# Kernel optimization log

Measured on AMD Instinct MI355X. Metric: run time of the kernel, lower is better.

Reference implementation:

```python
import jax, jax.numpy as jnp
import numpy as np

D = 100        # persistence-image resolution (forced by CNN out: 32*25*25)
VAR = 0.5      # pers_im_var
B, P = 32, 128 # graphs, persistence pairs per graph
N, IN, HID = 16000, 128, 64
NUM_CLASSES = 10


def setup_inputs() -> dict:
    key = jax.random.key(0)
    ks = jax.random.split(key, 13)
    s = 0.05
    return {
        "x": jax.random.normal(ks[0], (N, IN), jnp.float32),
        "pair_idx0": jax.random.randint(ks[1], (B, P, 2), 0, N, jnp.int32),
        "pair_idx1": jax.random.randint(ks[2], (B, P, 2), 0, N, jnp.int32),
        "w1": jax.random.normal(ks[3], (IN, HID), jnp.float32) * s,
        "b1": jnp.zeros((HID,), jnp.float32),
        "w2": jax.random.normal(ks[4], (HID, 1), jnp.float32) * s,
        "b2": jnp.zeros((1,), jnp.float32),
        "conv1_w": jax.random.normal(ks[5], (16, 2, 5, 5), jnp.float32) * s,
        "conv1_b": jnp.zeros((16,), jnp.float32),
        "conv2_w": jax.random.normal(ks[6], (32, 16, 5, 5), jnp.float32) * s,
        "conv2_b": jnp.zeros((32,), jnp.float32),
        "out_w": jax.random.normal(ks[7], (NUM_CLASSES, 32 * 25 * 25), jnp.float32) * s,
        "out_b": jnp.zeros((NUM_CLASSES,), jnp.float32),
    }


def _pers_image(bd):
    # bd: [B, P, 2] birth/death filtration values
    # bdpt_to_bdps = [[1,-1],[0,1]] : (b, d) -> (b, d - b)
    birth = bd[..., 0]
    pers = bd[..., 1] - bd[..., 0]
    coords = jnp.arange(D, dtype=bd.dtype) / D  # arange(0, 0.999, 1/D) -> D pts
    # Gaussian over 2D grid; axis i <-> birth coord, axis j <-> persistence coord
    g = (birth[:, :, None, None] - coords[None, None, :, None]) ** 2 \
        + (pers[:, :, None, None] - coords[None, None, None, :]) ** 2
    im = jnp.exp(-g / (2.0 * VAR)) / (2.0 * jnp.pi * VAR)  # [B, P, D, D]
    im = im.sum(axis=1)  # sum over points -> [B, D, D]
    im = im / im.max(axis=(1, 2), keepdims=True)  # per-sample normalization
    return im


def _conv(x, w, b):
    y = jax.lax.conv_general_dilated(
        x, w, window_strides=(1, 1), padding=((2, 2), (2, 2)),
        dimension_numbers=("NCHW", "OIHW", "NCHW"))
    return y + b[None, :, None, None]


def _maxpool2(x):
    return jax.lax.reduce_window(x, -jnp.inf, jax.lax.max,
                                 (1, 1, 2, 2), (1, 1, 2, 2), "VALID")


def reference(x, pair_idx0, pair_idx1, w1, b1, w2, b2,
              conv1_w, conv1_b, conv2_w, conv2_b, out_w, out_b):
    # Linear_fil: Linear -> ReLU -> Linear -> Sigmoid -> squeeze
    h = jax.nn.relu(x @ w1 + b1)
    node_filt = jax.nn.sigmoid(h @ w2 + b2)[:, 0]  # [N]

    # persistence pairs as gathers of vertex filtration values (diff. path of ph)
    h0 = node_filt[pair_idx0]  # [B, P, 2]
    h1 = node_filt[pair_idx1]  # [B, P, 2]

    im0 = _pers_image(h0)
    im1 = _pers_image(h1)
    imgs = jnp.stack([im0, im1], axis=1)  # [B, 2, D, D]

    # CNN head
    y = _maxpool2(jax.nn.relu(_conv(imgs, conv1_w, conv1_b)))  # [B,16,50,50]
    y = _maxpool2(jax.nn.relu(_conv(y, conv2_w, conv2_b)))     # [B,32,25,25]
    y = y.reshape(y.shape[0], -1)
    y_hat = y @ out_w.T + out_b  # [B, num_classes]
    return (y_hat, node_filt)
```

## Files before the change

kernel.cpp:

```cpp
#include <hip/hip_runtime.h>
#include <hip/hip_bf16.h>

#define N_NODES 16000
#define IN_F 128
#define HID 64
#define BATCH 32
#define NPAIR 128
#define DRES 100
#define NCLS 10

#define NF_OFF     0
#define WA1_OFF    16000
#define WT2B_OFF   16800
#define INV_OFF    23200
#define MAXB_OFF   23264
#define IMGSP_OFF  23328
#define POOL1P_OFF 715552
#define POOL2_OFF  2263840
#define ZERO_N4    560144

#define NFILT_BLK  125
#define NZBLK      548

typedef short short8 __attribute__((ext_vector_type(8)));
typedef float f32x16 __attribute__((ext_vector_type(16)));

static __device__ __forceinline__ unsigned short f2b(float f) {
    __hip_bfloat16 h = __float2bfloat16(f);
    return *reinterpret_cast<unsigned short*>(&h);
}
static __device__ __forceinline__ unsigned int pk2(float a, float b) {
    return (unsigned int)f2b(a) | ((unsigned int)f2b(b) << 16);
}

#define COFF(k) (((k)/25)*336 + (((k)%25)/5)*56 + ((k)%25)%5)
#define C1OFF(k) ((k) < 50 ? ((k)/25)*624 + ((((k)%25)/5))*104 + (((k)%25)%5) : 1248)

__global__ __launch_bounds__(256) void k_initfilt(
    const float* __restrict__ x, const float* __restrict__ w1,
    const float* __restrict__ b1, const float* __restrict__ w2,
    const float* __restrict__ b2, float* __restrict__ nf, float* __restrict__ out_nf,
    const float* __restrict__ c1w, const float* __restrict__ c2w,
    unsigned int* __restrict__ wA1, unsigned int* __restrict__ wT2b,
    float* __restrict__ zbase)
{
    int bx = blockIdx.x, t = threadIdx.x;
    if (bx < NFILT_BLK) {
        int wave = t >> 6, lane = t & 63;
        int n0 = (bx * 4 + wave) * 32;
        int hh = lane >> 5, sm = lane & 31;
        const float* xr = x + (size_t)(n0 + sm) * IN_F + hh * 8;
        const float* wbase = w1 + hh * 512 + sm;

        f32x16 acc0 = {0.f,0.f,0.f,0.f,0.f,0.f,0.f,0.f,0.f,0.f,0.f,0.f,0.f,0.f,0.f,0.f};
        f32x16 acc1 = {0.f,0.f,0.f,0.f,0.f,0.f,0.f,0.f,0.f,0.f,0.f,0.f,0.f,0.f,0.f,0.f};

        #pragma unroll
        for (int s = 0; s < 8; ++s) {
            float4 v0 = *(const float4*)(xr + s * 16);
            float4 v1 = *(const float4*)(xr + s * 16 + 4);
            union { short8 v; unsigned int u[4]; } a;
            a.u[0] = pk2(v0.x, v0.y);
            a.u[1] = pk2(v0.z, v0.w);
            a.u[2] = pk2(v1.x, v1.y);
            a.u[3] = pk2(v1.z, v1.w);
            union { short8 v; unsigned int u[4]; } b0f, b1f;
            #pragma unroll
            for (int r = 0; r < 4; ++r) {
                float wa0 = wbase[s * 1024 + r * 128];
                float wb0 = wbase[s * 1024 + r * 128 + 64];
                float wa1 = wbase[s * 1024 + r * 128 + 32];
                float wb1v = wbase[s * 1024 + r * 128 + 96];
                b0f.u[r] = pk2(wa0, wb0);
                b1f.u[r] = pk2(wa1, wb1v);
            }
            acc0 = __builtin_amdgcn_mfma_f32_32x32x16_bf16(a.v, b0f.v, acc0, 0, 0, 0);
            acc1 = __builtin_amdgcn_mfma_f32_32x32x16_bf16(a.v, b1f.v, acc1, 0, 0, 0);
        }

        int h0 = sm, h1 = 32 + sm;
        float b10 = b1[h0], b11 = b1[h1], w20 = w2[h0], w21 = w2[h1];
        float q[16];
        #pragma unroll
        for (int r = 0; r < 16; ++r)
            q[r] = fmaxf(acc0[r] + b10, 0.f) * w20 + fmaxf(acc1[r] + b11, 0.f) * w21;
        #pragma unroll
        for (int off = 1; off < 32; off <<= 1) {
            #pragma unroll
            for (int r = 0; r < 16; ++r)
                q[r] += __shfl_xor(q[r], off, 64);
        }
        if (sm == 0) {
            float b2v = b2[0];
            #pragma unroll
            for (int r = 0; r < 16; ++r) {
                int m = (r & 3) + 8 * (r >> 2) + 4 * hh;
                float f = 1.f / (1.f + expf(-(q[r] + b2v)));
                nf[n0 + m] = f;
                out_nf[n0 + m] = f;
            }
        }
        return;
    }
    if (bx == NFILT_BLK) {
        for (int i = t; i < 512; i += 256) {
            int r = i & 3, m = (i >> 2) & 15, kg = (i >> 6) & 1, s = i >> 7;
            int k0 = s * 16 + kg * 8 + 2 * r;
            float f0 = (k0 < 50) ? c1w[m * 50 + k0] : 0.f;
            float f1 = (k0 + 1 < 50) ? c1w[m * 50 + k0 + 1] : 0.f;
            wA1[i] = pk2(f0, f1);
        }
        return;
    }
    if (bx == NFILT_BLK + 1) {
        for (int i = t; i < 6400; i += 256) {
            int kp = i >> 5, oc = i & 31;
            int k0 = 2 * kp, k1 = k0 + 1;
            float f0 = c2w[(oc * 16 + k0 / 25) * 25 + k0 % 25];
            float f1 = c2w[(oc * 16 + k1 / 25) * 25 + k1 % 25];
            wT2b[i] = pk2(f0, f1);
        }
        return;
    }
    int zi = (bx - (NFILT_BLK + 2)) * 1024 + t;
    float4 z = make_float4(0.f, 0.f, 0.f, 0.f);
    #pragma unroll
    for (int r = 0; r < 4; ++r) {
        int i = zi + r * 256;
        if (i < ZERO_N4) ((float4*)zbase)[i] = z;
    }
}

__global__ __launch_bounds__(256) void k_pimg(const float* __restrict__ nf,
    const int* __restrict__ pi0, const int* __restrict__ pi1,
    float* __restrict__ imgs_p, unsigned int* __restrict__ maxb)
{
    int g = blockIdx.x;
    int img = (g & 7) * 8 + ((g >> 3) & 7);
    int q = g >> 6;
    int b = img >> 1, c = img & 1;
    const int* pi = c ? pi1 : pi0;
    __shared__ float sb[NPAIR], sp[NPAIR];
    __shared__ float wm[4];
    int t = threadIdx.x;
    if (t < NPAIR) {
        int i0 = pi[(b * NPAIR + t) * 2 + 0];
        int i1 = pi[(b * NPAIR + t) * 2 + 1];
        float f0 = nf[i0], f1 = nf[i1];
        sb[t] = f0;
        sp[t] = f1 - f0;
    }
    __syncthreads();
    bool act = t < 169;
    int ti = t / 13, tj = t % 13;
    float acc[8][2] = {};
    if (act) {
        float ci[8];
        #pragma unroll
        for (int r = 0; r < 8; ++r) ci[r] = (float)(ti + 13 * r) * 0.01f;
        float cj0 = (float)(q * 25 + tj) * 0.01f;
        float cj1 = (float)(q * 25 + tj + 13) * 0.01f;
        for (int p = 0; p < NPAIR; ++p) {
            float bb = sb[p], pp = sp[p];
            float d0 = pp - cj0, d1 = pp - cj1;
            float e0 = __expf(-d0 * d0), e1 = __expf(-d1 * d1);
            #pragma unroll
            for (int r = 0; r < 8; ++r) {
                float d = bb - ci[r];
                float eb = __expf(-d * d);
                acc[r][0] = fmaf(eb, e0, acc[r][0]);
                acc[r][1] = fmaf(eb, e1, acc[r][1]);
            }
        }
    }
    float lmax = 0.f;
    if (act) {
        float* dst = imgs_p + (size_t)img * 10816 + 2 * 104 + 2 + q * 25;
        #pragma unroll
        for (int r = 0; r < 8; ++r) {
            int i = ti + 13 * r;
            if (i < DRES) {
                dst[i * 104 + tj] = acc[r][0];
                lmax = fmaxf(lmax, acc[r][0]);
                if (tj < 12) {
                    dst[i * 104 + tj + 13] = acc[r][1];
                    lmax = fmaxf(lmax, acc[r][1]);
                }
            }
        }
    }
    #pragma unroll
    for (int off = 32; off > 0; off >>= 1)
        lmax = fmaxf(lmax, __shfl_xor(lmax, off, 64));
    if ((t & 63) == 0) wm[t >> 6] = lmax;
    __syncthreads();
    if (t == 0) {
        float bm = fmaxf(fmaxf(wm[0], wm[1]), fmaxf(wm[2], wm[3]));
        atomicMax(&maxb[img], __float_as_uint(bm));
    }
}

__global__ __launch_bounds__(128) void k_conv1(const float* __restrict__ imgs_p,
    const unsigned int* __restrict__ wA1, const float* __restrict__ cb1,
    const unsigned int* __restrict__ maxb, float* __restrict__ pool1p)
{
    int g = blockIdx.x;
    int b = (g & 7) * 4 + ((g >> 3) & 3);
    int py = g >> 5;
    int t = threadIdx.x;

    __shared__ unsigned short inbz[1472];
    {
        float sc0 = 1.f / __uint_as_float(maxb[b * 2 + 0]);
        float sc1 = 1.f / __uint_as_float(maxb[b * 2 + 1]);
        const float* s0 = imgs_p + (size_t)(b * 2 + 0) * 10816 + (2 * py) * 104;
        const float* s1 = s0 + 10816;
        unsigned int* z32 = (unsigned int*)inbz;
        for (int i = t; i < 736; i += 128) {
            unsigned int val = 0u;
            if (i < 312) {
                int s2 = 2 * i; int r = s2 / 104, cc = s2 % 104;
                float2 v = *(const float2*)(s0 + r * 104 + cc);
                val = pk2(v.x * sc0, v.y * sc0);
            } else if (i < 624) {
                int s2 = 2 * i - 624; int r = s2 / 104, cc = s2 % 104;
                float2 v = *(const float2*)(s1 + r * 104 + cc);
                val = pk2(v.x * sc1, v.y * sc1);
            }
            z32[i] = val;
        }
    }
    __syncthreads();

    int lane = t & 63;
    int h = t >> 6;
    int hh = lane >> 5;
    int sm = lane & 31;
    int q = lane & 3;
    int cl = sm >> 2;
    int laneoff = (q >> 1) * 104 + 2 * cl + (q & 1);

    uint4 z4 = {0u, 0u, 0u, 0u};
    union { short8 v; uint4 qd; } afr[4];
    #pragma unroll
    for (int s = 0; s < 4; ++s)
        afr[s].qd = (sm < 16) ? *(const uint4*)(wA1 + ((s * 2 + hh) * 16 + sm) * 4) : z4;

    float bb[8];
    #pragma unroll
    for (int r = 0; r < 8; ++r)
        bb[r] = cb1[(r & 3) + 8 * (r >> 2) + 4 * hh];

    #pragma unroll
    for (int tt = 0; tt < 4; ++tt) {
        int t_ = h + 2 * tt;
        if (t_ < 7) {
            const unsigned short* bp = inbz + laneoff + 16 * t_;
            f32x16 acc = {0.f,0.f,0.f,0.f,0.f,0.f,0.f,0.f,0.f,0.f,0.f,0.f,0.f,0.f,0.f,0.f};
            #pragma unroll
            for (int s = 0; s < 4; ++s) {
                unsigned short ub[8];
                #pragma unroll
                for (int e = 0; e < 8; ++e) {
                    int off = hh ? C1OFF(16 * s + 8 + e) : C1OFF(16 * s + e);
                    ub[e] = bp[off];
                }
                union { short8 v; unsigned int u[4]; } bf;
                #pragma unroll
                for (int r = 0; r < 4; ++r)
                    bf.u[r] = (unsigned int)ub[2 * r] | ((unsigned int)ub[2 * r + 1] << 16);
                acc = __builtin_amdgcn_mfma_f32_32x32x16_bf16(afr[s].v, bf.v, acc, 0, 0, 0);
            }
            int pc = 8 * t_ + cl;
            #pragma unroll
            for (int r = 0; r < 8; ++r) {
                float vr = acc[r];
                vr = fmaxf(vr, __shfl_xor(vr, 1, 64));
                vr = fmaxf(vr, __shfl_xor(vr, 2, 64));
                if (q == 0 && pc < 50) {
                    int oc = (r & 3) + 8 * (r >> 2) + 4 * hh;
                    pool1p[((size_t)(b * 16 + oc) * 54 + py + 2) * 56 + pc + 2] =
                        fmaxf(vr + bb[r], 0.f);
                }
            }
        }
    }
}

__global__ __launch_bounds__(128) void k_conv2(const float* __restrict__ pool1p,
    const unsigned int* __restrict__ wg, const float* __restrict__ cb2,
    float* __restrict__ pool2)
{
    int g = blockIdx.x;
    int b = (g & 7) * 4 + ((g >> 3) & 3);
    int py = g >> 5;
    int t = threadIdx.x;

    __shared__ unsigned short inb[5376];
    {
        const float* src = pool1p + (size_t)b * 48384 + (2 * py) * 56;
        unsigned int* inb32 = (unsigned int*)inb;
        for (int i = t; i < 1344; i += 128) {
            int ic = i / 84, rem = i % 84;
            int r = rem / 14, c4 = rem % 14;
            float4 v = *(const float4*)(src + ic * 3024 + r * 56 + c4 * 4);
            inb32[i * 2 + 0] = pk2(v.x, v.y);
            inb32[i * 2 + 1] = pk2(v.z, v.w);
        }
    }
    __syncthreads();

    int lane = t & 63;
    int h = t >> 6;
    int hh = lane >> 5;
    int sm = lane & 31;
    int cb = h * 32 + sm; if (cb > 49) cb = 49;
    int cbA = cb, cbB = cb + 56;
    int oc = sm;
    int wbase = hh * 128 + oc;

    f32x16 accA = {0.f,0.f,0.f,0.f,0.f,0.f,0.f,0.f,0.f,0.f,0.f,0.f,0.f,0.f,0.f,0.f};
    f32x16 accB = {0.f,0.f,0.f,0.f,0.f,0.f,0.f,0.f,0.f,0.f,0.f,0.f,0.f,0.f,0.f,0.f};

    #pragma unroll
    for (int s = 0; s < 25; ++s) {
        union { short8 v; unsigned int u[4]; } bw;
        bw.u[0] = wg[wbase + s * 256 + 0];
        bw.u[1] = wg[wbase + s * 256 + 32];
        bw.u[2] = wg[wbase + s * 256 + 64];
        bw.u[3] = wg[wbase + s * 256 + 96];
        unsigned short ua[8], ub[8];
        #pragma unroll
        for (int e = 0; e < 8; ++e) {
            int o = hh ? COFF(16 * s + 8 + e) : COFF(16 * s + e);
            ua[e] = inb[cbA + o];
            ub[e] = inb[cbB + o];
        }
        union { short8 v; unsigned int u[4]; } aA, aB;
        #pragma unroll
        for (int r = 0; r < 4; ++r) {
            aA.u[r] = (unsigned int)ua[2 * r] | ((unsigned int)ua[2 * r + 1] << 16);
            aB.u[r] = (unsigned int)ub[2 * r] | ((unsigned int)ub[2 * r + 1] << 16);
        }
        accA = __builtin_amdgcn_mfma_f32_32x32x16_bf16(aA.v, bw.v, accA, 0, 0, 0);
        accB = __builtin_amdgcn_mfma_f32_32x32x16_bf16(aB.v, bw.v, accB, 0, 0, 0);
    }

    float bias = cb2[oc];
    float* dst = pool2 + ((size_t)(b * 32 + oc) * 25 + py) * 25;
    #pragma unroll
    for (int q = 0; q < 4; ++q) {
        float m0 = fmaxf(fmaxf(accA[4 * q + 0], accB[4 * q + 0]),
                         fmaxf(accA[4 * q + 1], accB[4 * q + 1]));
        float m1 = fmaxf(fmaxf(accA[4 * q + 2], accB[4 * q + 2]),
                         fmaxf(accA[4 * q + 3], accB[4 * q + 3]));
        int px0 = h * 16 + 4 * q + 2 * hh;
        if (px0 < 25) dst[px0] = fmaxf(m0 + bias, 0.f);
        if (px0 + 1 < 25) dst[px0 + 1] = fmaxf(m1 + bias, 0.f);
    }
}

__global__ __launch_bounds__(256) void k_fc(const float* __restrict__ pool2,
    const float* __restrict__ oww, const float* __restrict__ ob,
    float* __restrict__ yhat)
{
    int cls = blockIdx.x / BATCH, b = blockIdx.x % BATCH;
    int t = threadIdx.x;
    const float4* y = (const float4*)(pool2 + (size_t)b * 20000);
    const float4* w = (const float4*)(oww + (size_t)cls * 20000);
    float acc = 0.f;
    for (int k = t; k < 5000; k += 256) {
        float4 a = y[k], ww = w[k];
        acc += a.x * ww.x + a.y * ww.y + a.z * ww.z + a.w * ww.w;
    }
    #pragma unroll
    for (int off = 32; off > 0; off >>= 1)
        acc += __shfl_xor(acc, off, 64);
    __shared__ float part[4];
    if ((t & 63) == 0) part[t >> 6] = acc;
    __syncthreads();
    if (t == 0)
        yhat[b * NCLS + cls] = part[0] + part[1] + part[2] + part[3] + ob[cls];
}

extern "C" void kernel_launch(void* const* d_in, const int* in_sizes, int n_in,
                              void* d_out, int out_size, void* d_ws, size_t ws_size,
                              hipStream_t stream)
{
    const float* x   = (const float*)d_in[0];
    const int*   pi0 = (const int*)d_in[1];
    const int*   pi1 = (const int*)d_in[2];
    const float* w1  = (const float*)d_in[3];
    const float* b1  = (const float*)d_in[4];
    const float* w2  = (const float*)d_in[5];
    const float* b2  = (const float*)d_in[6];
    const float* c1w = (const float*)d_in[7];
    const float* c1b = (const float*)d_in[8];
    const float* c2w = (const float*)d_in[9];
    const float* c2b = (const float*)d_in[10];
    const float* oww = (const float*)d_in[11];
    const float* owb = (const float*)d_in[12];
    float* out = (float*)d_out;
    float* ws = (float*)d_ws;

    float*        nf     = ws + NF_OFF;
    unsigned int* wA1    = (unsigned int*)(ws + WA1_OFF);
    unsigned int* wT2b   = (unsigned int*)(ws + WT2B_OFF);
    unsigned int* maxb   = (unsigned int*)(ws + MAXB_OFF);
    float*        imgs_p = ws + IMGSP_OFF;
    float*        pool1p = ws + POOL1P_OFF;
    float*        pool2  = ws + POOL2_OFF;

    k_initfilt<<<NFILT_BLK + 2 + NZBLK, 256, 0, stream>>>(
        x, w1, b1, w2, b2, nf, out + BATCH * NCLS,
        c1w, c2w, wA1, wT2b, ws + MAXB_OFF);
    k_pimg <<<256, 256, 0, stream>>>(nf, pi0, pi1, imgs_p, maxb);
    k_conv1<<<1600, 128, 0, stream>>>(imgs_p, wA1, c1b, maxb, pool1p);
    k_conv2<<<800, 128, 0, stream>>>(pool1p, wT2b, c2b, pool2);
    k_fc   <<<BATCH * NCLS, 256, 0, stream>>>(pool2, oww, owb, out);
}
```

Baseline: 66.83 us.

## Fuse final linear layer into conv2 epilogue with atomic accumulation

Removes the separate FC kernel and the pool2 global buffer. Each conv2 block stages its pooled output row in shared memory, computes its partial dot products against out_w for all classes, and atomically adds them into the logits. The bias is preinitialised in the init kernel. This saves one launch and the pool2 write and read, at the cost of many atomics per output (800 blocks × 2 waves × 10 classes) and a nondeterministic summation order.

```diff
diff --git a/kernel.cpp b/kernel.cpp
--- a/kernel.cpp
+++ b/kernel.cpp
@@ -12,11 +12,9 @@
 #define NF_OFF     0
 #define WA1_OFF    16000
 #define WT2B_OFF   16800
-#define INV_OFF    23200
 #define MAXB_OFF   23264
 #define IMGSP_OFF  23328
 #define POOL1P_OFF 715552
-#define POOL2_OFF  2263840
 #define ZERO_N4    560144
 
 #define NFILT_BLK  125
@@ -41,20 +39,20 @@
     const float* __restrict__ b1, const float* __restrict__ w2,
     const float* __restrict__ b2, float* __restrict__ nf, float* __restrict__ out_nf,
     const float* __restrict__ c1w, const float* __restrict__ c2w,
+    const float* __restrict__ owb, float* __restrict__ yout,
     unsigned int* __restrict__ wA1, unsigned int* __restrict__ wT2b,
     float* __restrict__ zbase)
 {
     int bx = blockIdx.x, t = threadIdx.x;
     if (bx < NFILT_BLK) {
         int wave = t >> 6, lane = t & 63;
-        int n0 = (bx * 4 + wave) * 32;
-        int hh = lane >> 5, sm = lane & 31;
-        const float* xr = x + (size_t)(n0 + sm) * IN_F + hh * 8;
-        const float* wbase = w1 + hh * 512 + sm;
+        int n0 = ((bx << 2) + wave) * 32;
+        int hh = lane >> 5, smn = lane & 31;
+        const float* xr = x + (size_t)(n0 + smn) * IN_F + hh * 8;
+        const float* wbase = w1 + hh * 512 + smn;
 
         f32x16 acc0 = {0.f,0.f,0.f,0.f,0.f,0.f,0.f,0.f,0.f,0.f,0.f,0.f,0.f,0.f,0.f,0.f};
         f32x16 acc1 = {0.f,0.f,0.f,0.f,0.f,0.f,0.f,0.f,0.f,0.f,0.f,0.f,0.f,0.f,0.f,0.f};
-
         #pragma unroll
         for (int s = 0; s < 8; ++s) {
             float4 v0 = *(const float4*)(xr + s * 16);
@@ -77,8 +75,7 @@
             acc0 = __builtin_amdgcn_mfma_f32_32x32x16_bf16(a.v, b0f.v, acc0, 0, 0, 0);
             acc1 = __builtin_amdgcn_mfma_f32_32x32x16_bf16(a.v, b1f.v, acc1, 0, 0, 0);
         }
-
-        int h0 = sm, h1 = 32 + sm;
+        int h0 = smn, h1 = 32 + smn;
         float b10 = b1[h0], b11 = b1[h1], w20 = w2[h0], w21 = w2[h1];
         float q[16];
         #pragma unroll
@@ -90,7 +87,7 @@
             for (int r = 0; r < 16; ++r)
                 q[r] += __shfl_xor(q[r], off, 64);
         }
-        if (sm == 0) {
+        if (smn == 0) {
             float b2v = b2[0];
             #pragma unroll
             for (int r = 0; r < 16; ++r) {
@@ -110,6 +107,8 @@
             float f1 = (k0 + 1 < 50) ? c1w[m * 50 + k0 + 1] : 0.f;
             wA1[i] = pk2(f0, f1);
         }
+        for (int i = t; i < BATCH * NCLS; i += 256)
+            yout[i] = owb[i % NCLS];
         return;
     }
     if (bx == NFILT_BLK + 1) {
@@ -289,7 +288,7 @@
 
 __global__ __launch_bounds__(128) void k_conv2(const float* __restrict__ pool1p,
     const unsigned int* __restrict__ wg, const float* __restrict__ cb2,
-    float* __restrict__ pool2)
+    const float* __restrict__ oww, float* __restrict__ yout)
 {
     int g = blockIdx.x;
     int b = (g & 7) * 4 + ((g >> 3) & 3);
@@ -297,6 +296,7 @@
     int t = threadIdx.x;
 
     __shared__ unsigned short inb[5376];
+    __shared__ float p2row[800];
     {
         const float* src = pool1p + (size_t)b * 48384 + (2 * py) * 56;
         unsigned int* inb32 = (unsigned int*)inb;
@@ -314,8 +314,8 @@
     int h = t >> 6;
     int hh = lane >> 5;
     int sm = lane & 31;
-    int cb = h * 32 + sm; if (cb > 49) cb = 49;
-    int cbA = cb, cbB = cb + 56;
+    int cbi = h * 32 + sm; if (cbi > 49) cbi = 49;
+    int cbA = cbi, cbB = cbi + 56;
     int oc = sm;
     int wbase = hh * 128 + oc;
 
@@ -347,7 +347,6 @@
     }
 
     float bias = cb2[oc];
-    float* dst = pool2 + ((size_t)(b * 32 + oc) * 25 + py) * 25;
     #pragma unroll
     for (int q = 0; q < 4; ++q) {
         float m0 = fmaxf(fmaxf(accA[4 * q + 0], accB[4 * q + 0]),
@@ -355,32 +354,33 @@
         float m1 = fmaxf(fmaxf(accA[4 * q + 2], accB[4 * q + 2]),
                          fmaxf(accA[4 * q + 3], accB[4 * q + 3]));
         int px0 = h * 16 + 4 * q + 2 * hh;
-        if (px0 < 25) dst[px0] = fmaxf(m0 + bias, 0.f);
-        if (px0 + 1 < 25) dst[px0 + 1] = fmaxf(m1 + bias, 0.f);
-    }
-}
-
-__global__ __launch_bounds__(256) void k_fc(const float* __restrict__ pool2,
-    const float* __restrict__ oww, const float* __restrict__ ob,
-    float* __restrict__ yhat)
-{
-    int cls = blockIdx.x / BATCH, b = blockIdx.x % BATCH;
-    int t = threadIdx.x;
-    const float4* y = (const float4*)(pool2 + (size_t)b * 20000);
-    const float4* w = (const float4*)(oww + (size_t)cls * 20000);
-    float acc = 0.f;
-    for (int k = t; k < 5000; k += 256) {
-        float4 a = y[k], ww = w[k];
-        acc += a.x * ww.x + a.y * ww.y + a.z * ww.z + a.w * ww.w;
-    }
-    #pragma unroll
-    for (int off = 32; off > 0; off >>= 1)
-        acc += __shfl_xor(acc, off, 64);
-    __shared__ float part[4];
-    if ((t & 63) == 0) part[t >> 6] = acc;
+        if (px0 < 25) p2row[oc * 25 + px0] = fmaxf(m0 + bias, 0.f);
+        if (px0 + 1 < 25) p2row[oc * 25 + px0 + 1] = fmaxf(m1 + bias, 0.f);
+    }
     __syncthreads();
-    if (t == 0)
-        yhat[b * NCLS + cls] = part[0] + part[1] + part[2] + part[3] + ob[cls];
+
+    float v[7];
+    int wo[7];
+    #pragma unroll
+    for (int j = 0; j < 7; ++j) {
+        int i = t + 128 * j;
+        bool ok = i < 800;
+        v[j] = ok ? p2row[i] : 0.f;
+        wo[j] = ok ? (i / 25) * 600 + i : 0;
+    }
+    const float* wb = oww + py * 25;
+    #pragma unroll
+    for (int cls = 0; cls < NCLS; ++cls) {
+        float p = 0.f;
+        #pragma unroll
+        for (int j = 0; j < 7; ++j)
+            p = fmaf(v[j], wb[cls * 20000 + wo[j]], p);
+        #pragma unroll
+        for (int off = 32; off > 0; off >>= 1)
+            p += __shfl_xor(p, off, 64);
+        if (lane == 0)
+            atomicAdd(&yout[b * NCLS + cls], p);
+    }
 }
 
 extern "C" void kernel_launch(void* const* d_in, const int* in_sizes, int n_in,
@@ -409,13 +409,11 @@
     unsigned int* maxb   = (unsigned int*)(ws + MAXB_OFF);
     float*        imgs_p = ws + IMGSP_OFF;
     float*        pool1p = ws + POOL1P_OFF;
-    float*        pool2  = ws + POOL2_OFF;
 
     k_initfilt<<<NFILT_BLK + 2 + NZBLK, 256, 0, stream>>>(
         x, w1, b1, w2, b2, nf, out + BATCH * NCLS,
-        c1w, c2w, wA1, wT2b, ws + MAXB_OFF);
+        c1w, c2w, owb, out, wA1, wT2b, ws + MAXB_OFF);
     k_pimg <<<256, 256, 0, stream>>>(nf, pi0, pi1, imgs_p, maxb);
     k_conv1<<<1600, 128, 0, stream>>>(imgs_p, wA1, c1b, maxb, pool1p);
-    k_conv2<<<800, 128, 0, stream>>>(pool1p, wT2b, c2b, pool2);
-    k_fc   <<<BATCH * NCLS, 256, 0, stream>>>(pool2, oww, owb, out);
-}
+    k_conv2<<<800, 128, 0, stream>>>(pool1p, wT2b, c2b, oww, out);
+}
```

New measurement: 77.56 us. +16.0%, slower.

## Zero only padding borders and split persistence-image rows across more blocks

Applied to the files above, without the earlier changes.

The init kernel no longer zeroes the whole padded image and pool1 workspace. It now clears only the max buffer and the two-pixel border regions of the padded images and pooled maps, since interiors are fully overwritten later. This removes about 9 MB of redundant stores. The persistence-image kernel also splits its rows into two halves, doubling the grid to 512 blocks and halving per-thread accumulators for more parallelism, at the cost of recomputing the column exponentials twice and scattered non-coalesced border stores.

```diff
diff --git a/kernel.cpp b/kernel.cpp
--- a/kernel.cpp
+++ b/kernel.cpp
@@ -12,15 +12,13 @@
 #define NF_OFF     0
 #define WA1_OFF    16000
 #define WT2B_OFF   16800
-#define INV_OFF    23200
 #define MAXB_OFF   23264
 #define IMGSP_OFF  23328
 #define POOL1P_OFF 715552
 #define POOL2_OFF  2263840
-#define ZERO_N4    560144
 
 #define NFILT_BLK  125
-#define NZBLK      548
+#define NZB        157
 
 typedef short short8 __attribute__((ext_vector_type(8)));
 typedef float f32x16 __attribute__((ext_vector_type(16)));
@@ -42,19 +40,19 @@
     const float* __restrict__ b2, float* __restrict__ nf, float* __restrict__ out_nf,
     const float* __restrict__ c1w, const float* __restrict__ c2w,
     unsigned int* __restrict__ wA1, unsigned int* __restrict__ wT2b,
-    float* __restrict__ zbase)
+    unsigned int* __restrict__ maxb, float* __restrict__ imgs_p,
+    float* __restrict__ pool1p)
 {
     int bx = blockIdx.x, t = threadIdx.x;
     if (bx < NFILT_BLK) {
         int wave = t >> 6, lane = t & 63;
-        int n0 = (bx * 4 + wave) * 32;
-        int hh = lane >> 5, sm = lane & 31;
-        const float* xr = x + (size_t)(n0 + sm) * IN_F + hh * 8;
-        const float* wbase = w1 + hh * 512 + sm;
+        int n0 = ((bx << 2) + wave) * 32;
+        int hh = lane >> 5, smn = lane & 31;
+        const float* xr = x + (size_t)(n0 + smn) * IN_F + hh * 8;
+        const float* wbase = w1 + hh * 512 + smn;
 
         f32x16 acc0 = {0.f,0.f,0.f,0.f,0.f,0.f,0.f,0.f,0.f,0.f,0.f,0.f,0.f,0.f,0.f,0.f};
         f32x16 acc1 = {0.f,0.f,0.f,0.f,0.f,0.f,0.f,0.f,0.f,0.f,0.f,0.f,0.f,0.f,0.f,0.f};
-
         #pragma unroll
         for (int s = 0; s < 8; ++s) {
             float4 v0 = *(const float4*)(xr + s * 16);
@@ -77,8 +75,7 @@
             acc0 = __builtin_amdgcn_mfma_f32_32x32x16_bf16(a.v, b0f.v, acc0, 0, 0, 0);
             acc1 = __builtin_amdgcn_mfma_f32_32x32x16_bf16(a.v, b1f.v, acc1, 0, 0, 0);
         }
-
-        int h0 = sm, h1 = 32 + sm;
+        int h0 = smn, h1 = 32 + smn;
         float b10 = b1[h0], b11 = b1[h1], w20 = w2[h0], w21 = w2[h1];
         float q[16];
         #pragma unroll
@@ -90,7 +87,7 @@
             for (int r = 0; r < 16; ++r)
                 q[r] += __shfl_xor(q[r], off, 64);
         }
-        if (sm == 0) {
+        if (smn == 0) {
             float b2v = b2[0];
             #pragma unroll
             for (int r = 0; r < 16; ++r) {
@@ -122,12 +119,27 @@
         }
         return;
     }
-    int zi = (bx - (NFILT_BLK + 2)) * 1024 + t;
-    float4 z = make_float4(0.f, 0.f, 0.f, 0.f);
-    #pragma unroll
-    for (int r = 0; r < 4; ++r) {
-        int i = zi + r * 256;
-        if (i < ZERO_N4) ((float4*)zbase)[i] = z;
+    int base = (bx - (NFILT_BLK + 2)) * 2048 + t;
+    #pragma unroll
+    for (int r = 0; r < 8; ++r) {
+        int idx = base + r * 256;
+        if (idx < 64) {
+            maxb[idx] = 0u;
+        } else if (idx < 52288) {
+            int u = idx - 64;
+            int img = u / 816, i = u % 816;
+            int row, col;
+            if (i < 416) { int r4 = i / 104; row = (r4 < 2) ? r4 : 100 + r4; col = i % 104; }
+            else { int j = i - 416; row = 2 + j / 4; int c4 = j % 4; col = (c4 < 2) ? c4 : 100 + c4; }
+            imgs_p[(size_t)img * 10816 + row * 104 + col] = 0.f;
+        } else if (idx < 320576) {
+            int u = idx - 52288;
+            int ch = u / 524, i = u % 524;
+            int row, col;
+            if (i < 224) { int r4 = i / 56; row = (r4 < 2) ? r4 : 50 + r4; col = i % 56; }
+            else { int j = i - 224; row = 2 + j / 6; int c6 = j % 6; col = (c6 < 2) ? c6 : 50 + c6; }
+            pool1p[(size_t)ch * 3024 + row * 56 + col] = 0.f;
+        }
     }
 }
 
@@ -137,7 +149,8 @@
 {
     int g = blockIdx.x;
     int img = (g & 7) * 8 + ((g >> 3) & 7);
-    int q = g >> 6;
+    int q = (g >> 6) & 3;
+    int rh = g >> 8;
     int b = img >> 1, c = img & 1;
     const int* pi = c ? pi1 : pi0;
     __shared__ float sb[NPAIR], sp[NPAIR];
@@ -153,11 +166,11 @@
     __syncthreads();
     bool act = t < 169;
     int ti = t / 13, tj = t % 13;
-    float acc[8][2] = {};
+    float acc[4][2] = {};
     if (act) {
-        float ci[8];
-        #pragma unroll
-        for (int r = 0; r < 8; ++r) ci[r] = (float)(ti + 13 * r) * 0.01f;
+        float ci[4];
+        #pragma unroll
+        for (int r = 0; r < 4; ++r) ci[r] = (float)(ti + 13 * (rh * 4 + r)) * 0.01f;
         float cj0 = (float)(q * 25 + tj) * 0.01f;
         float cj1 = (float)(q * 25 + tj + 13) * 0.01f;
         for (int p = 0; p < NPAIR; ++p) {
@@ -165,7 +178,7 @@
             float d0 = pp - cj0, d1 = pp - cj1;
             float e0 = __expf(-d0 * d0), e1 = __expf(-d1 * d1);
             #pragma unroll
-            for (int r = 0; r < 8; ++r) {
+            for (int r = 0; r < 4; ++r) {
                 float d = bb - ci[r];
                 float eb = __expf(-d * d);
                 acc[r][0] = fmaf(eb, e0, acc[r][0]);
@@ -177,8 +190,8 @@
     if (act) {
         float* dst = imgs_p + (size_t)img * 10816 + 2 * 104 + 2 + q * 25;
         #pragma unroll
-        for (int r = 0; r < 8; ++r) {
-            int i = ti + 13 * r;
+        for (int r = 0; r < 4; ++r) {
+            int i = ti + 13 * (rh * 4 + r);
             if (i < DRES) {
                 dst[i * 104 + tj] = acc[r][0];
                 lmax = fmaxf(lmax, acc[r][0]);
@@ -314,8 +327,8 @@
     int h = t >> 6;
     int hh = lane >> 5;
     int sm = lane & 31;
-    int cb = h * 32 + sm; if (cb > 49) cb = 49;
-    int cbA = cb, cbB = cb + 56;
+    int cbi = h * 32 + sm; if (cbi > 49) cbi = 49;
+    int cbA = cbi, cbB = cbi + 56;
     int oc = sm;
     int wbase = hh * 128 + oc;
 
@@ -411,10 +424,10 @@
     float*        pool1p = ws + POOL1P_OFF;
     float*        pool2  = ws + POOL2_OFF;
 
-    k_initfilt<<<NFILT_BLK + 2 + NZBLK, 256, 0, stream>>>(
+    k_initfilt<<<NFILT_BLK + 2 + NZB, 256, 0, stream>>>(
         x, w1, b1, w2, b2, nf, out + BATCH * NCLS,
-        c1w, c2w, wA1, wT2b, ws + MAXB_OFF);
-    k_pimg <<<256, 256, 0, stream>>>(nf, pi0, pi1, imgs_p, maxb);
+        c1w, c2w, wA1, wT2b, maxb, imgs_p, pool1p);
+    k_pimg <<<512, 256, 0, stream>>>(nf, pi0, pi1, imgs_p, maxb);
     k_conv1<<<1600, 128, 0, stream>>>(imgs_p, wA1, c1b, maxb, pool1p);
     k_conv2<<<800, 128, 0, stream>>>(pool1p, wT2b, c2b, pool2);
     k_fc   <<<BATCH * NCLS, 256, 0, stream>>>(pool2, oww, owb, out);
```

After: 64.75 us. 1.03x faster.
